# Optimization experiments

Hardware: AMD Instinct MI355X
Metric: run time of the kernel (lower is better)

## Reference

```python
import jax, jax.numpy as jnp
import numpy as np

B = 64          # num_graphs per batch
ADJ = 1000      # adj_shape (nodes per graph)
N = B * ADJ     # total nodes
E = 1 << 20     # edges
M = 32000       # selected (batch, node) pairs
D_IN = 128
D_OUT = 128


def setup_inputs() -> dict:
    key = jax.random.key(0)
    ks = jax.random.split(key, 12)
    inp = {
        "x0": jax.random.normal(ks[0], (N, D_IN), jnp.float32),
        "x1": jax.random.normal(ks[1], (N, D_IN), jnp.float32),
        "edge_index": jax.random.randint(ks[2], (2, E), 0, N, jnp.int64),
        "b_idx0": jax.random.randint(ks[3], (M,), 0, B, jnp.int64),
        "n_idx0": jax.random.randint(ks[4], (M,), 0, ADJ, jnp.int64),
        "b_idx1": jax.random.randint(ks[5], (M,), 0, B, jnp.int64),
        "n_idx1": jax.random.randint(ks[6], (M,), 0, ADJ, jnp.int64),
        "W1": jax.random.normal(ks[7], (D_IN, D_IN), jnp.float32) / np.sqrt(D_IN),
        "b1": jnp.zeros((D_IN,), jnp.float32),
        "W2": jax.random.normal(ks[8], (D_IN, D_IN), jnp.float32) / np.sqrt(D_IN),
        "b2": jnp.zeros((D_IN,), jnp.float32),
        "Wl": jax.random.normal(ks[9], (D_IN, D_OUT), jnp.float32) / np.sqrt(D_IN),
        "bl": jnp.zeros((D_OUT,), jnp.float32),
        "Wfi": jax.random.normal(ks[10], (D_IN, D_OUT), jnp.float32) / np.sqrt(D_IN),
        "bfi": jnp.zeros((D_OUT,), jnp.float32),
    }
    return inp


def _gnn_layer(h, edge_index, W, b):
    # GCN-style message passing: gather source features, scatter-sum to dst,
    # then linear project.  h: [N, d]
    msgs = h[edge_index[0]]                                    # [E, d] gather
    agg = jax.ops.segment_sum(msgs, edge_index[1], num_segments=N)  # [N, d]
    return agg @ W + b


def reference(x0, x1, edge_index, b_idx0, n_idx0, b_idx1, n_idx1,
              W1, b1, W2, b2, Wl, bl, Wfi, bfi):
    # branch i == 0: raw features -> 2D gather -> fc_in
    d0 = x0.reshape(B, ADJ, -1)[b_idx0, n_idx0]                # [M, D_IN]
    d0 = d0 @ Wfi + bfi                                        # [M, D_OUT]

    # branch i == 1 (observ=True): gnn1 -> gnn2 -> 2D gather -> linear
    # (dropout omitted for deterministic reference; p=0.2 at train time)
    h = _gnn_layer(x1, edge_index, W1, b1)
    h = _gnn_layer(h, edge_index, W2, b2)
    d1 = h.reshape(B, ADJ, -1)[b_idx1, n_idx1]                 # [M, D_IN]
    d1 = d1 @ Wl + bl                                          # [M, D_OUT]

    return jnp.stack([d0, d1])                                 # [2, M, D_OUT]
```

## Files before the change

### kernel.cpp

```cpp
#include <hip/hip_runtime.h>
#include <hip/hip_bf16.h>


#define B_    64
#define ADJ_  1000
#define N_    64000
#define E_    (1 << 20)
#define M_    32000
#define DV    128
#define CAP   64
#define RANGES 8
#define RSPAN  (N_ / RANGES)
#define CHUNKS 512
#define EPB    (E_ / CHUNKS)

typedef __attribute__((ext_vector_type(8))) short short8v;
typedef __attribute__((ext_vector_type(4))) float float4v;

__device__ __forceinline__ float u2f(unsigned int u) {
  union { unsigned int i; float f; } x; x.i = u; return x.f;
}
__device__ __forceinline__ unsigned short f2bf(float f) {
  union { float f; unsigned int i; } x; x.f = f;
  unsigned int r = x.i + 0x7fffu + ((x.i >> 16) & 1u);
  return (unsigned short)(r >> 16);
}
__device__ __forceinline__ unsigned int pack_bf2(float a, float b) {
  __hip_bfloat162 h = __float22bfloat162_rn(float2{a, b});
  union { __hip_bfloat162 h; unsigned int u; } c; c.h = h;
  return c.u;
}

__global__ __launch_bounds__(256)
void prep_k(const float* __restrict__ W1, const float* __restrict__ Wfi,
            const float* __restrict__ W2, const float* __restrict__ Wl,
            unsigned short* __restrict__ Wbf, int* __restrict__ counts) {
  int b = blockIdx.x, t = threadIdx.x;
  int mi = b >> 3;
  const float* W = (mi == 0) ? W1 : (mi == 1) ? Wfi : (mi == 2) ? W2 : Wl;
  unsigned short* out = Wbf + mi * 16384;
  int base = (b & 7) * 2048 + t * 8;
  float4 f0 = *(const float4*)(W + base);
  float4 f1 = *(const float4*)(W + base + 4);
  float v[8] = {f0.x, f0.y, f0.z, f0.w, f1.x, f1.y, f1.z, f1.w};
#pragma unroll
  for (int u = 0; u < 8; u++) {
    int g = base + u;
    int k = g >> 7, n = g & 127;
    int addr = ((((n >> 4) * 4 + (k >> 5)) * 64 + ((k >> 3) & 3) * 16 + (n & 15)) << 3)
             + (k & 7);
    out[addr] = f2bf(v[u]);
  }
  for (int i = b * 256 + t; i < N_; i += 32 * 256) counts[i] = 0;
}

__device__ __forceinline__ void fill_part(const int* __restrict__ ei,
                                          int* __restrict__ counts,
                                          unsigned short* __restrict__ bucket,
                                          int c, int r) {
  const int* srcA = ei;
  const int* dstA = ei + E_;
  int lo = r * RSPAN;
  int t4 = c * EPB + (int)threadIdx.x * 4;
  int4 d0 = *(const int4*)(dstA + t4);
  int4 s0 = *(const int4*)(srcA + t4);
  int4 d1 = *(const int4*)(dstA + t4 + 1024);
  int4 s1 = *(const int4*)(srcA + t4 + 1024);
#define PROC(D, S) do {                                                \
    if ((unsigned)((D) - lo) < (unsigned)RSPAN) {                      \
      int pos = atomicAdd(&counts[(D)], 1);                            \
      if (pos < CAP) bucket[(D) * CAP + pos] = (unsigned short)(S);    \
    } } while (0)
  PROC(d0.x, s0.x); PROC(d0.y, s0.y); PROC(d0.z, s0.z); PROC(d0.w, s0.w);
  PROC(d1.x, s1.x); PROC(d1.y, s1.y); PROC(d1.z, s1.z); PROC(d1.w, s1.w);
#undef PROC
}

template<bool GATHER, bool ABF16, bool OUTBF16, bool HASBIAS>
__device__ __forceinline__ void gemm_tile(const void* __restrict__ in,
                                          const unsigned short* __restrict__ Wbf,
                                          const float* __restrict__ bias,
                                          void* __restrict__ out_, int tile,
                                          const int* __restrict__ bidx,
                                          const int* __restrict__ nidx,
                                          unsigned short* __restrict__ Bs) {
  int tid  = threadIdx.x;
  int lane = tid & 63;
  int wv   = tid >> 6;
  int m    = lane & 15;
  int q    = lane >> 4;
  int rbase = tile * 64 + wv * 16;
  int r     = rbase + m;

  const short8v* Wv  = (const short8v*)Wbf;
  short8v*       Bsv = (short8v*)Bs;

  short8v w[4];
#pragma unroll
  for (int i = 0; i < 4; i++) w[i] = Wv[tid + i * 256];

  size_t ir;
  if (GATHER) ir = (size_t)bidx[r] * ADJ_ + nidx[r];
  else        ir = (size_t)r;

  short8v af[4];
  if (ABF16) {
    const unsigned short* arow = (const unsigned short*)in + ir * DV;
#pragma unroll
    for (int kc = 0; kc < 4; kc++)
      af[kc] = *(const short8v*)(arow + kc * 32 + q * 8);
  } else {
    const float* arow = (const float*)in + ir * DV;
#pragma unroll
    for (int kc = 0; kc < 4; kc++) {
      const float4* p = (const float4*)(arow + kc * 32 + q * 8);
      float4 f0 = p[0], f1 = p[1];
      union { short8v s; unsigned int u[4]; } t;
      t.u[0] = pack_bf2(f0.x, f0.y);
      t.u[1] = pack_bf2(f0.z, f0.w);
      t.u[2] = pack_bf2(f1.x, f1.y);
      t.u[3] = pack_bf2(f1.z, f1.w);
      af[kc] = t.s;
    }
  }

#pragma unroll
  for (int i = 0; i < 4; i++) Bsv[tid + i * 256] = w[i];
  __syncthreads();

  float4v acc[8];
#pragma unroll
  for (int nb = 0; nb < 8; nb++) acc[nb] = (float4v){0.f, 0.f, 0.f, 0.f};

#pragma unroll
  for (int i = 0; i < 4; i++) w[i] = Wv[1024 + tid + i * 256];

#pragma unroll
  for (int nb = 0; nb < 4; nb++)
#pragma unroll
    for (int kc = 0; kc < 4; kc++) {
      short8v bf = Bsv[(nb * 4 + kc) * 64 + lane];
      acc[nb] = __builtin_amdgcn_mfma_f32_16x16x32_bf16(af[kc], bf, acc[nb], 0, 0, 0);
    }
  __syncthreads();
#pragma unroll
  for (int i = 0; i < 4; i++) Bsv[tid + i * 256] = w[i];
  __syncthreads();
#pragma unroll
  for (int nb = 4; nb < 8; nb++)
#pragma unroll
    for (int kc = 0; kc < 4; kc++) {
      short8v bf = Bsv[((nb - 4) * 4 + kc) * 64 + lane];
      acc[nb] = __builtin_amdgcn_mfma_f32_16x16x32_bf16(af[kc], bf, acc[nb], 0, 0, 0);
    }

#pragma unroll
  for (int nb = 0; nb < 8; nb++) {
    float bvn = HASBIAS ? bias[nb * 16 + m] : 0.f;
    int col = nb * 16 + m;
#pragma unroll
    for (int i = 0; i < 4; i++) {
      int row = rbase + q * 4 + i;
      float v = acc[nb][i] + bvn;
      if (OUTBF16) ((unsigned short*)out_)[(size_t)row * DV + col] = f2bf(v);
      else         ((float*)out_)[(size_t)row * DV + col] = v;
    }
  }
}

__global__ __launch_bounds__(256)
void k1_fused(const int* __restrict__ ei, int* __restrict__ counts,
              unsigned short* __restrict__ bucket,
              const float* __restrict__ x1, const unsigned short* __restrict__ Wbf,
              unsigned int* __restrict__ t_bf,
              const float* __restrict__ x0, const float* __restrict__ bfi,
              float* __restrict__ out0,
              const int* __restrict__ b0, const int* __restrict__ n0i) {
  __shared__ unsigned short Bs[8192];
  int g = blockIdx.x >> 4, rem = blockIdx.x & 15;
  if (rem < 8) { fill_part(ei, counts, bucket, g, rem); return; }
  int o = g * 8 + rem - 8;
  if (o < 1000)
    gemm_tile<false, false, true, false>(x1, Wbf, nullptr, t_bf, o, nullptr, nullptr, Bs);
  else if (o < 1500)
    gemm_tile<true, false, false, true>(x0, Wbf + 16384, bfi, out0, o - 1000, b0, n0i, Bs);
}

template<bool GATHER, bool ABF16, bool OUTBF16, bool HASBIAS>
__global__ __launch_bounds__(256)
void gemm_k(const void* __restrict__ in, const unsigned short* __restrict__ Wbf,
            const float* __restrict__ bias, void* __restrict__ out_,
            const int* __restrict__ bidx, const int* __restrict__ nidx) {
  __shared__ unsigned short Bs[8192];
  gemm_tile<GATHER, ABF16, OUTBF16, HASBIAS>(in, Wbf, bias, out_, blockIdx.x, bidx, nidx, Bs);
}

template<bool OUTBF16, bool SEL>
__global__ __launch_bounds__(256)
void aggregate_k(const unsigned int* __restrict__ x,
                 const int* __restrict__ counts,
                 const unsigned short* __restrict__ bucket,
                 const float* __restrict__ bias, void* __restrict__ out_,
                 const int* __restrict__ bidx, const int* __restrict__ nidx) {
  int w    = (blockIdx.x * 256 + threadIdx.x) >> 6;
  int lane = threadIdx.x & 63;
  int node = SEL ? (bidx[w] * ADJ_ + nidx[w]) : w;
  int cnt = counts[node]; cnt = min(cnt, CAP);
  int mysrc = (int)bucket[node * CAP + lane];
  float2 bv = ((const float2*)bias)[lane];
  float2 acc; acc.x = bv.x; acc.y = bv.y;

  int d = 0;
  for (; d + 8 <= cnt; d += 8) {
    int s0 = __shfl(mysrc, d,     64);
    int s1 = __shfl(mysrc, d + 1, 64);
    int s2 = __shfl(mysrc, d + 2, 64);
    int s3 = __shfl(mysrc, d + 3, 64);
    int s4 = __shfl(mysrc, d + 4, 64);
    int s5 = __shfl(mysrc, d + 5, 64);
    int s6 = __shfl(mysrc, d + 6, 64);
    int s7 = __shfl(mysrc, d + 7, 64);
    unsigned int u0 = x[(size_t)s0 * 64 + lane];
    unsigned int u1 = x[(size_t)s1 * 64 + lane];
    unsigned int u2 = x[(size_t)s2 * 64 + lane];
    unsigned int u3 = x[(size_t)s3 * 64 + lane];
    unsigned int u4 = x[(size_t)s4 * 64 + lane];
    unsigned int u5 = x[(size_t)s5 * 64 + lane];
    unsigned int u6 = x[(size_t)s6 * 64 + lane];
    unsigned int u7 = x[(size_t)s7 * 64 + lane];
    acc.x += ((u2f(u0 << 16) + u2f(u1 << 16)) + (u2f(u2 << 16) + u2f(u3 << 16)))
           + ((u2f(u4 << 16) + u2f(u5 << 16)) + (u2f(u6 << 16) + u2f(u7 << 16)));
    acc.y += ((u2f(u0 & 0xffff0000u) + u2f(u1 & 0xffff0000u))
            + (u2f(u2 & 0xffff0000u) + u2f(u3 & 0xffff0000u)))
           + ((u2f(u4 & 0xffff0000u) + u2f(u5 & 0xffff0000u))
            + (u2f(u6 & 0xffff0000u) + u2f(u7 & 0xffff0000u)));
  }
  if (d + 4 <= cnt) {
    int s0 = __shfl(mysrc, d,     64);
    int s1 = __shfl(mysrc, d + 1, 64);
    int s2 = __shfl(mysrc, d + 2, 64);
    int s3 = __shfl(mysrc, d + 3, 64);
    unsigned int u0 = x[(size_t)s0 * 64 + lane];
    unsigned int u1 = x[(size_t)s1 * 64 + lane];
    unsigned int u2 = x[(size_t)s2 * 64 + lane];
    unsigned int u3 = x[(size_t)s3 * 64 + lane];
    acc.x += (u2f(u0 << 16) + u2f(u1 << 16)) + (u2f(u2 << 16) + u2f(u3 << 16));
    acc.y += (u2f(u0 & 0xffff0000u) + u2f(u1 & 0xffff0000u))
           + (u2f(u2 & 0xffff0000u) + u2f(u3 & 0xffff0000u));
    d += 4;
  }
  for (; d < cnt; d++) {
    int s = __shfl(mysrc, d, 64);
    unsigned int u = x[(size_t)s * 64 + lane];
    acc.x += u2f(u << 16);
    acc.y += u2f(u & 0xffff0000u);
  }
  if (OUTBF16) ((unsigned int*)out_)[(size_t)w * 64 + lane] = pack_bf2(acc.x, acc.y);
  else         ((float2*)out_)[(size_t)w * 64 + lane] = acc;
}

extern "C" void kernel_launch(void* const* d_in, const int* in_sizes, int n_in,
                              void* d_out, int out_size, void* d_ws, size_t ws_size,
                              hipStream_t stream) {
  const float* x0  = (const float*)d_in[0];
  const float* x1  = (const float*)d_in[1];
  const int*   ei  = (const int*)  d_in[2];
  const int*   b0  = (const int*)  d_in[3];
  const int*   n0i = (const int*)  d_in[4];
  const int*   b1  = (const int*)  d_in[5];
  const int*   n1i = (const int*)  d_in[6];
  const float* W1  = (const float*)d_in[7];
  const float* bb1 = (const float*)d_in[8];
  const float* W2  = (const float*)d_in[9];
  const float* bb2 = (const float*)d_in[10];
  const float* Wl  = (const float*)d_in[11];
  const float* bl  = (const float*)d_in[12];
  const float* Wfi = (const float*)d_in[13];
  const float* bfi = (const float*)d_in[14];
  float* out = (float*)d_out;

  unsigned int*   t_bf   = (unsigned int*)d_ws;
  unsigned int*   h_bf   = t_bf + (size_t)N_ * 64;
  unsigned int*   sel_bf = h_bf + (size_t)N_ * 64;
  int*            counts = (int*)(sel_bf + (size_t)M_ * 64);
  unsigned short* bucket = (unsigned short*)(counts + N_);
  unsigned short* Wbf    = bucket + (size_t)N_ * CAP;

  prep_k<<<32, 256, 0, stream>>>(W1, Wfi, W2, Wl, Wbf, counts);

  k1_fused<<<512 * 16, 256, 0, stream>>>(ei, counts, bucket, x1, Wbf, t_bf,
                                         x0, bfi, out, b0, n0i);

  aggregate_k<true, false><<<N_ / 4, 256, 0, stream>>>(t_bf, counts, bucket, bb1,
                                                       h_bf, nullptr, nullptr);
  gemm_k<false, true, true, false><<<N_ / 64, 256, 0, stream>>>(h_bf, Wbf + 2 * 16384,
                                                                nullptr, t_bf,
                                                                nullptr, nullptr);
  aggregate_k<true, true><<<M_ / 4, 256, 0, stream>>>(t_bf, counts, bucket, bb2,
                                                      sel_bf, b1, n1i);
  gemm_k<false, true, false, true><<<M_ / 64, 256, 0, stream>>>(sel_bf, Wbf + 3 * 16384,
                                                                bl, out + (size_t)M_ * DV,
                                                                nullptr, nullptr);
}
```

Before: 262.5 us.

## Fold W2 into Wl, single-pass bucket fill, batched aggregate loads

Precomputes W2·Wl and b2·Wl+bl in the prep kernel. This drops the full N-row GEMM after the first aggregation, so the second aggregation gathers h directly and feeds one combined GEMM over the selected rows. Bucket filling now does a single pass per edge chunk with 32-bit relaxed atomic stores, instead of eight range-filtered passes with 16-bit stores, and the fill and GEMM blocks are interleaved through a bitmask. The aggregate loop issues 16 gathers at a time with predicated accumulation to raise memory-level parallelism. The costs are a doubled bucket footprint, extra gathered loads past the edge count, and unordered atomic placement of bucket entries.

Result: slower. 268.0 us (+2.1%).

```diff
diff --git a/kernel.cpp b/kernel.cpp
--- a/kernel.cpp
+++ b/kernel.cpp
@@ -9,10 +9,9 @@
 #define M_    32000
 #define DV    128
 #define CAP   64
-#define RANGES 8
-#define RSPAN  (N_ / RANGES)
 #define CHUNKS 512
-#define EPB    (E_ / CHUNKS)
+#define EPB   (E_ / CHUNKS)
+#define FMASK 0x18844221u
 
 typedef __attribute__((ext_vector_type(8))) short short8v;
 typedef __attribute__((ext_vector_type(4))) float float4v;
@@ -31,46 +30,67 @@
   return c.u;
 }
 
+__device__ __forceinline__ int frag_addr(int k, int n) {
+  return ((((n >> 4) * 4 + (k >> 5)) * 64 + ((k >> 3) & 3) * 16 + (n & 15)) << 3)
+       + (k & 7);
+}
+
 __global__ __launch_bounds__(256)
 void prep_k(const float* __restrict__ W1, const float* __restrict__ Wfi,
             const float* __restrict__ W2, const float* __restrict__ Wl,
-            unsigned short* __restrict__ Wbf, int* __restrict__ counts) {
+            const float* __restrict__ b2, const float* __restrict__ bl,
+            unsigned short* __restrict__ Wbf, float* __restrict__ bc,
+            int* __restrict__ counts) {
   int b = blockIdx.x, t = threadIdx.x;
-  int mi = b >> 3;
-  const float* W = (mi == 0) ? W1 : (mi == 1) ? Wfi : (mi == 2) ? W2 : Wl;
-  unsigned short* out = Wbf + mi * 16384;
-  int base = (b & 7) * 2048 + t * 8;
-  float4 f0 = *(const float4*)(W + base);
-  float4 f1 = *(const float4*)(W + base + 4);
-  float v[8] = {f0.x, f0.y, f0.z, f0.w, f1.x, f1.y, f1.z, f1.w};
-#pragma unroll
-  for (int u = 0; u < 8; u++) {
-    int g = base + u;
-    int k = g >> 7, n = g & 127;
-    int addr = ((((n >> 4) * 4 + (k >> 5)) * 64 + ((k >> 3) & 3) * 16 + (n & 15)) << 3)
-             + (k & 7);
-    out[addr] = f2bf(v[u]);
+  if (b < 16) {
+    const float* W = (b < 8) ? W1 : Wfi;
+    unsigned short* out = Wbf + ((b < 8) ? 0 : 16384);
+    int base = (b & 7) * 2048 + t * 8;
+    float4 f0 = *(const float4*)(W + base);
+    float4 f1 = *(const float4*)(W + base + 4);
+    float v[8] = {f0.x, f0.y, f0.z, f0.w, f1.x, f1.y, f1.z, f1.w};
+#pragma unroll
+    for (int u = 0; u < 8; u++) {
+      int g = base + u;
+      out[frag_addr(g >> 7, g & 127)] = f2bf(v[u]);
+    }
+  } else if (b < 48) {
+    unsigned short* out = Wbf + 2 * 16384;
+    int g0 = (b - 16) * 512 + t * 2;
+#pragma unroll
+    for (int u = 0; u < 2; u++) {
+      int g = g0 + u, k = g >> 7, n = g & 127;
+      float acc = 0.f;
+      for (int j = 0; j < 128; j++) acc += W2[k * 128 + j] * Wl[j * 128 + n];
+      out[frag_addr(k, n)] = f2bf(acc);
+    }
+  } else {
+    if (t < 128) {
+      float acc = bl[t];
+      for (int k = 0; k < 128; k++) acc += b2[k] * Wl[k * 128 + t];
+      bc[t] = acc;
+    }
   }
-  for (int i = b * 256 + t; i < N_; i += 32 * 256) counts[i] = 0;
-}
-
-__device__ __forceinline__ void fill_part(const int* __restrict__ ei,
+  for (int i = b * 256 + t; i < N_; i += 49 * 256) counts[i] = 0;
+}
+
+__device__ __forceinline__ void fill_once(const int* __restrict__ ei,
                                           int* __restrict__ counts,
-                                          unsigned short* __restrict__ bucket,
-                                          int c, int r) {
+                                          unsigned int* __restrict__ bucket,
+                                          int c) {
   const int* srcA = ei;
   const int* dstA = ei + E_;
-  int lo = r * RSPAN;
   int t4 = c * EPB + (int)threadIdx.x * 4;
   int4 d0 = *(const int4*)(dstA + t4);
   int4 s0 = *(const int4*)(srcA + t4);
   int4 d1 = *(const int4*)(dstA + t4 + 1024);
   int4 s1 = *(const int4*)(srcA + t4 + 1024);
-#define PROC(D, S) do {                                                \
-    if ((unsigned)((D) - lo) < (unsigned)RSPAN) {                      \
-      int pos = atomicAdd(&counts[(D)], 1);                            \
-      if (pos < CAP) bucket[(D) * CAP + pos] = (unsigned short)(S);    \
-    } } while (0)
+#define PROC(D, S) do {                                                         \
+    int pos = atomicAdd(&counts[(D)], 1);                                       \
+    if (pos < CAP)                                                              \
+      __hip_atomic_store(&bucket[(size_t)(D) * CAP + pos], (unsigned int)(S),   \
+                         __ATOMIC_RELAXED, __HIP_MEMORY_SCOPE_AGENT);           \
+  } while (0)
   PROC(d0.x, s0.x); PROC(d0.y, s0.y); PROC(d0.z, s0.z); PROC(d0.w, s0.w);
   PROC(d1.x, s1.x); PROC(d1.y, s1.y); PROC(d1.z, s1.z); PROC(d1.w, s1.w);
 #undef PROC
@@ -170,16 +190,17 @@
 
 __global__ __launch_bounds__(256)
 void k1_fused(const int* __restrict__ ei, int* __restrict__ counts,
-              unsigned short* __restrict__ bucket,
+              unsigned int* __restrict__ bucket,
               const float* __restrict__ x1, const unsigned short* __restrict__ Wbf,
               unsigned int* __restrict__ t_bf,
               const float* __restrict__ x0, const float* __restrict__ bfi,
               float* __restrict__ out0,
               const int* __restrict__ b0, const int* __restrict__ n0i) {
   __shared__ unsigned short Bs[8192];
-  int g = blockIdx.x >> 4, rem = blockIdx.x & 15;
-  if (rem < 8) { fill_part(ei, counts, bucket, g, rem); return; }
-  int o = g * 8 + rem - 8;
+  unsigned int rem = blockIdx.x & 31, hi = blockIdx.x >> 5;
+  int below = __popc(FMASK & ((1u << rem) - 1u));
+  if ((FMASK >> rem) & 1u) { fill_once(ei, counts, bucket, hi * 8 + below); return; }
+  int o = hi * 24 + (int)(rem - below);
   if (o < 1000)
     gemm_tile<false, false, true, false>(x1, Wbf, nullptr, t_bf, o, nullptr, nullptr, Bs);
   else if (o < 1500)
@@ -199,62 +220,40 @@
 __global__ __launch_bounds__(256)
 void aggregate_k(const unsigned int* __restrict__ x,
                  const int* __restrict__ counts,
-                 const unsigned short* __restrict__ bucket,
+                 const unsigned int* __restrict__ bucket,
                  const float* __restrict__ bias, void* __restrict__ out_,
                  const int* __restrict__ bidx, const int* __restrict__ nidx) {
   int w    = (blockIdx.x * 256 + threadIdx.x) >> 6;
   int lane = threadIdx.x & 63;
   int node = SEL ? (bidx[w] * ADJ_ + nidx[w]) : w;
   int cnt = counts[node]; cnt = min(cnt, CAP);
-  int mysrc = (int)bucket[node * CAP + lane];
-  float2 bv = ((const float2*)bias)[lane];
-  float2 acc; acc.x = bv.x; acc.y = bv.y;
-
-  int d = 0;
-  for (; d + 8 <= cnt; d += 8) {
-    int s0 = __shfl(mysrc, d,     64);
-    int s1 = __shfl(mysrc, d + 1, 64);
-    int s2 = __shfl(mysrc, d + 2, 64);
-    int s3 = __shfl(mysrc, d + 3, 64);
-    int s4 = __shfl(mysrc, d + 4, 64);
-    int s5 = __shfl(mysrc, d + 5, 64);
-    int s6 = __shfl(mysrc, d + 6, 64);
-    int s7 = __shfl(mysrc, d + 7, 64);
-    unsigned int u0 = x[(size_t)s0 * 64 + lane];
-    unsigned int u1 = x[(size_t)s1 * 64 + lane];
-    unsigned int u2 = x[(size_t)s2 * 64 + lane];
-    unsigned int u3 = x[(size_t)s3 * 64 + lane];
-    unsigned int u4 = x[(size_t)s4 * 64 + lane];
-    unsigned int u5 = x[(size_t)s5 * 64 + lane];
-    unsigned int u6 = x[(size_t)s6 * 64 + lane];
-    unsigned int u7 = x[(size_t)s7 * 64 + lane];
-    acc.x += ((u2f(u0 << 16) + u2f(u1 << 16)) + (u2f(u2 << 16) + u2f(u3 << 16)))
-           + ((u2f(u4 << 16) + u2f(u5 << 16)) + (u2f(u6 << 16) + u2f(u7 << 16)));
-    acc.y += ((u2f(u0 & 0xffff0000u) + u2f(u1 & 0xffff0000u))
-            + (u2f(u2 & 0xffff0000u) + u2f(u3 & 0xffff0000u)))
-           + ((u2f(u4 & 0xffff0000u) + u2f(u5 & 0xffff0000u))
-            + (u2f(u6 & 0xffff0000u) + u2f(u7 & 0xffff0000u)));
-  }
-  if (d + 4 <= cnt) {
-    int s0 = __shfl(mysrc, d,     64);
-    int s1 = __shfl(mysrc, d + 1, 64);
-    int s2 = __shfl(mysrc, d + 2, 64);
-    int s3 = __shfl(mysrc, d + 3, 64);
-    unsigned int u0 = x[(size_t)s0 * 64 + lane];
-    unsigned int u1 = x[(size_t)s1 * 64 + lane];
-    unsigned int u2 = x[(size_t)s2 * 64 + lane];
-    unsigned int u3 = x[(size_t)s3 * 64 + lane];
-    acc.x += (u2f(u0 << 16) + u2f(u1 << 16)) + (u2f(u2 << 16) + u2f(u3 << 16));
-    acc.y += (u2f(u0 & 0xffff0000u) + u2f(u1 & 0xffff0000u))
-           + (u2f(u2 & 0xffff0000u) + u2f(u3 & 0xffff0000u));
-    d += 4;
-  }
-  for (; d < cnt; d++) {
-    int s = __shfl(mysrc, d, 64);
-    unsigned int u = x[(size_t)s * 64 + lane];
-    acc.x += u2f(u << 16);
-    acc.y += u2f(u & 0xffff0000u);
-  }
+  int mysrc = (int)bucket[(size_t)node * CAP + lane];
+
+  float2 acc;
+  if (bias) { float2 bv = ((const float2*)bias)[lane]; acc.x = bv.x; acc.y = bv.y; }
+  else      { acc.x = 0.f; acc.y = 0.f; }
+
+#define BATCH16(BASE) do {                                               \
+    unsigned int uu[16];                                                 \
+    _Pragma("unroll")                                                    \
+    for (int i = 0; i < 16; i++) {                                       \
+      int s = __shfl(mysrc, (BASE) + i, 64) & 0xffff;                    \
+      uu[i] = x[(size_t)s * 64 + lane];                                  \
+    }                                                                    \
+    _Pragma("unroll")                                                    \
+    for (int i = 0; i < 16; i++) {                                       \
+      unsigned int mm = ((BASE) + i < cnt) ? uu[i] : 0u;                 \
+      acc.x += u2f(mm << 16);                                            \
+      acc.y += u2f(mm & 0xffff0000u);                                    \
+    }                                                                    \
+  } while (0)
+
+  BATCH16(0);
+  if (cnt > 16) BATCH16(16);
+  if (cnt > 32) BATCH16(32);
+  if (cnt > 48) BATCH16(48);
+#undef BATCH16
+
   if (OUTBF16) ((unsigned int*)out_)[(size_t)w * 64 + lane] = pack_bf2(acc.x, acc.y);
   else         ((float2*)out_)[(size_t)w * 64 + lane] = acc;
 }
@@ -280,25 +279,23 @@
   float* out = (float*)d_out;
 
   unsigned int*   t_bf   = (unsigned int*)d_ws;
+  unsigned int*   sel_bf = t_bf;
   unsigned int*   h_bf   = t_bf + (size_t)N_ * 64;
-  unsigned int*   sel_bf = h_bf + (size_t)N_ * 64;
-  int*            counts = (int*)(sel_bf + (size_t)M_ * 64);
-  unsigned short* bucket = (unsigned short*)(counts + N_);
-  unsigned short* Wbf    = bucket + (size_t)N_ * CAP;
-
-  prep_k<<<32, 256, 0, stream>>>(W1, Wfi, W2, Wl, Wbf, counts);
-
-  k1_fused<<<512 * 16, 256, 0, stream>>>(ei, counts, bucket, x1, Wbf, t_bf,
-                                         x0, bfi, out, b0, n0i);
-
-  aggregate_k<true, false><<<N_ / 4, 256, 0, stream>>>(t_bf, counts, bucket, bb1,
-                                                       h_bf, nullptr, nullptr);
-  gemm_k<false, true, true, false><<<N_ / 64, 256, 0, stream>>>(h_bf, Wbf + 2 * 16384,
-                                                                nullptr, t_bf,
+  int*            counts = (int*)(h_bf + (size_t)N_ * 64);
+  unsigned int*   bucket = (unsigned int*)(counts + N_);
+  unsigned short* Wbf    = (unsigned short*)(bucket + (size_t)N_ * CAP);
+  float*          bc     = (float*)(Wbf + 3 * 16384);
+
+  prep_k<<<49, 256, 0, stream>>>(W1, Wfi, W2, Wl, bb2, bl, Wbf, bc, counts);
+
+  k1_fused<<<2048, 256, 0, stream>>>(ei, counts, bucket, x1, Wbf, t_bf,
+                                     x0, bfi, out, b0, n0i);
+
+  aggregate_k<true, false><<<N_ / 4, 256, 0, stream>>>(t_bf, counts, bucket,
+                                                       bb1, h_bf, nullptr, nullptr);
+  aggregate_k<true, true><<<M_ / 4, 256, 0, stream>>>(h_bf, counts, bucket,
+                                                      nullptr, sel_bf, b1, n1i);
+  gemm_k<false, true, false, true><<<M_ / 64, 256, 0, stream>>>(sel_bf, Wbf + 2 * 16384,
+                                                                bc, out + (size_t)M_ * DV,
                                                                 nullptr, nullptr);
-  aggregate_k<true, true><<<M_ / 4, 256, 0, stream>>>(t_bf, counts, bucket, bb2,
-                                                      sel_bf, b1, n1i);
-  gemm_k<false, true, false, true><<<M_ / 64, 256, 0, stream>>>(sel_bf, Wbf + 3 * 16384,
-                                                                bl, out + (size_t)M_ * DV,
-                                                                nullptr, nullptr);
-}
+}
```
